# Optimization experiments

Hardware: AMD Instinct MI355X
Metric: run time of the kernel (lower is better)

Reference implementation:

```python
import jax, jax.numpy as jnp
import numpy as np

N, E, H, L, IN, OUT = 50000, 800000, 64, 14, 128, 112
MSG_EPS = 1e-7   # GENConv message epsilon
LN_EPS = 1e-5    # torch.nn.LayerNorm default eps


def setup_inputs() -> dict:
    key = jax.random.key(0)
    ks = jax.random.split(key, 8)
    s = 0.05
    x = jax.random.normal(ks[0], (N, IN), jnp.float32)
    edge_index = jax.random.randint(ks[1], (2, E), 0, N, dtype=jnp.int64)
    enc_W = jax.random.normal(ks[2], (IN, H), jnp.float32) * s
    enc_b = jnp.zeros((H,), jnp.float32)
    ln_g = jnp.ones((L, H), jnp.float32)
    ln_b = jnp.zeros((L, H), jnp.float32)
    mlp_W = jax.random.normal(ks[3], (L, H, H), jnp.float32) * s
    mlp_b = jnp.zeros((L, H), jnp.float32)
    pred_W = jax.random.normal(ks[4], (H, OUT), jnp.float32) * s
    pred_b = jnp.zeros((OUT,), jnp.float32)
    return dict(x=x, edge_index=edge_index, enc_W=enc_W, enc_b=enc_b,
                ln_g=ln_g, ln_b=ln_b, mlp_W=mlp_W, mlp_b=mlp_b,
                pred_W=pred_W, pred_b=pred_b)


def _layernorm(h, g, b):
    mu = jnp.mean(h, axis=-1, keepdims=True)
    var = jnp.mean(jnp.square(h - mu), axis=-1, keepdims=True)  # biased, as torch
    return (h - mu) * jax.lax.rsqrt(var + LN_EPS) * g + b


def _genconv(h, src, dst, W, b):
    # GENConv: msg = relu(x_src) + eps; softmax aggregation (t=1) over dst; out = Linear(x + agg)
    msg = jax.nn.relu(h[src]) + MSG_EPS                    # [E, H]
    mmax = jax.ops.segment_max(msg, dst, num_segments=N)   # [N, H]
    mmax = jnp.where(jnp.isfinite(mmax), mmax, 0.0)         # empty segments
    ex = jnp.exp(msg - mmax[dst])                           # [E, H]
    denom = jax.ops.segment_sum(ex, dst, num_segments=N)    # [N, H]
    num = jax.ops.segment_sum(msg * ex, dst, num_segments=N)
    agg = num / jnp.maximum(denom, 1e-16)                   # 0 for isolated nodes
    return (h + agg) @ W + b


def reference(x, edge_index, enc_W, enc_b, ln_g, ln_b, mlp_W, mlp_b, pred_W, pred_b):
    src, dst = edge_index[0], edge_index[1]
    h = x @ enc_W + enc_b                       # node feature encoder
    h = _genconv(h, src, dst, mlp_W[0], mlp_b[0])  # first GCN (no pre-norm in res+)

    def body(h, params):
        g, bl, W, b = params
        h2 = jax.nn.relu(_layernorm(h, g, bl))  # dropout is identity (eval)
        h = _genconv(h2, src, dst, W, b) + h    # residual
        return h, None

    h, _ = jax.lax.scan(body, h, (ln_g[:L - 1], ln_b[:L - 1], mlp_W[1:], mlp_b[1:]))
    return h @ pred_W + pred_b
```

## Files before the change

### kernel.cpp

```cpp
#include <hip/hip_runtime.h>
#include <hip/hip_bf16.h>

#define NN 50000
#define EE 800000
#define HD 64
#define LL 14
#define IND 128
#define OUTD 112
#define LN2 0.69314718056f

typedef __attribute__((ext_vector_type(8))) short short8;
typedef __attribute__((ext_vector_type(4))) float float4_;
typedef __attribute__((ext_vector_type(4))) unsigned short ushort4_;

__device__ __forceinline__ short bf16_hi(float x) {
    return (short)(__float_as_uint(x) >> 16);
}
__device__ __forceinline__ float bf16_f(short s) {
    return __uint_as_float(((unsigned)(unsigned short)s) << 16);
}
__device__ __forceinline__ float us2f(unsigned short u) {
    return __uint_as_float(((unsigned)u) << 16);
}
__device__ __forceinline__ unsigned short f2b_rne(float x) {
    unsigned u = __float_as_uint(x);
    u += 0x7fffu + ((u >> 16) & 1u);
    return (unsigned short)(u >> 16);
}

__device__ __forceinline__ void split8(const float* p, short8& hi, short8& lo) {
    float4_ a = *(const float4_*)p;
    float4_ b = *(const float4_*)(p + 4);
    float v[8] = {a[0], a[1], a[2], a[3], b[0], b[1], b[2], b[3]};
    #pragma unroll
    for (int j = 0; j < 8; ++j) {
        short h = bf16_hi(v[j]);
        hi[j] = h;
        lo[j] = bf16_hi(v[j] - bf16_f(h));
    }
}

__device__ __forceinline__ void load_b(const float* __restrict__ W, int ldw,
                                       int colbase, int krow, short8& hi, short8& lo) {
    #pragma unroll
    for (int j = 0; j < 8; ++j) {
        float wv = W[(krow + j) * ldw + colbase];
        short h = bf16_hi(wv);
        hi[j] = h;
        lo[j] = bf16_hi(wv - bf16_f(h));
    }
}

__device__ __forceinline__ float4_ mm3(short8 ah, short8 al, short8 bh, short8 bl,
                                       float4_ acc) {
    acc = __builtin_amdgcn_mfma_f32_16x16x32_bf16(ah, bh, acc, 0, 0, 0);
    acc = __builtin_amdgcn_mfma_f32_16x16x32_bf16(al, bh, acc, 0, 0, 0);
    acc = __builtin_amdgcn_mfma_f32_16x16x32_bf16(ah, bl, acc, 0, 0, 0);
    return acc;
}


__global__ void k_hist(const int* __restrict__ ei, int* __restrict__ cnt,
                       int* __restrict__ rank) {
    int e = blockIdx.x * blockDim.x + threadIdx.x;
    if (e < EE) rank[e] = atomicAdd(&cnt[ei[EE + e]], 1);
}

__global__ __launch_bounds__(1024) void k_scan1(const int* __restrict__ deg,
                                                int* __restrict__ excl,
                                                int* __restrict__ bsum) {
    __shared__ int ws[16];
    int tid = threadIdx.x, lane = tid & 63, w = tid >> 6;
    int gid = blockIdx.x * 1024 + tid;
    int v = (gid < NN) ? deg[gid] : 0;
    int x = v;
    #pragma unroll
    for (int d = 1; d < 64; d <<= 1) {
        int y = __shfl_up(x, d);
        if (lane >= d) x += y;
    }
    if (lane == 63) ws[w] = x;
    __syncthreads();
    if (tid == 0) {
        int acc = 0;
        for (int i = 0; i < 16; i++) { int t = ws[i]; ws[i] = acc; acc += t; }
        bsum[blockIdx.x] = acc;
    }
    __syncthreads();
    if (gid < NN) excl[gid] = x - v + ws[w];
}

__global__ void k_scan2(const int* __restrict__ bsum, int* __restrict__ boff, int nb) {
    if (threadIdx.x == 0) {
        int acc = 0;
        for (int i = 0; i < nb; i++) { boff[i] = acc; acc += bsum[i]; }
    }
}

__global__ __launch_bounds__(1024) void k_scan3(int* __restrict__ rp,
                                                const int* __restrict__ boff) {
    int gid = blockIdx.x * 1024 + threadIdx.x;
    if (gid < NN) rp[gid] += boff[blockIdx.x];
    if (gid == 0) rp[NN] = EE;
}

__global__ void k_scatter(const int* __restrict__ ei, const int* __restrict__ rp,
                          const int* __restrict__ rank, int* __restrict__ csrc) {
    int e = blockIdx.x * blockDim.x + threadIdx.x;
    if (e < EE) {
        int d = ei[EE + e];
        csrc[rp[d] + rank[e]] = ei[e];
    }
}


__global__ __launch_bounds__(256) void k_enc(const float* __restrict__ x,
                                             const float* __restrict__ W,
                                             const float* __restrict__ b,
                                             float* __restrict__ h,
                                             unsigned short* __restrict__ P0) {
    __shared__ float X[16 * 132];
    int tid = threadIdx.x, lane = tid & 63, w = tid >> 6;
    int nb = blockIdx.x * 16;
    int nq = lane >> 4, nr = lane & 15;
    int colbase = w * 16 + nr;

    {
        const float* src = x + (size_t)nb * IND + tid * 8;
        float4_ a = *(const float4_*)src;
        float4_ c = *(const float4_*)(src + 4);
        int m = tid >> 4, k8 = 8 * (tid & 15);
        *(float4_*)&X[m * 132 + k8] = a;
        *(float4_*)&X[m * 132 + k8 + 4] = c;
    }
    __syncthreads();

    float4_ acc = {};
    #pragma unroll
    for (int t = 0; t < 4; ++t) {
        short8 ah, al, bh, bl;
        split8(&X[nr * 132 + t * 32 + nq * 8], ah, al);
        load_b(W, HD, colbase, t * 32 + nq * 8, bh, bl);
        acc = mm3(ah, al, bh, bl, acc);
    }

    float bias = b[colbase];
    #pragma unroll
    for (int r = 0; r < 4; ++r) {
        int node = nb + nq * 4 + r;
        float y = acc[r] + bias;
        h[node * HD + colbase] = y;
        float msg = fminf(fmaxf(y, 0.f) + 1e-7f, 50.f);
        P0[node * HD + colbase] = f2b_rne(__expf(msg));
    }
}


__global__ __launch_bounds__(256) void k_layer(const unsigned short* __restrict__ Pin,
                                               const float* __restrict__ selfh,
                                               const float* __restrict__ hres,
                                               float* __restrict__ hout,
                                               unsigned short* __restrict__ Pout,
                                               const int* __restrict__ rp,
                                               const int* __restrict__ csrc,
                                               const float* __restrict__ W,
                                               const float* __restrict__ b,
                                               const float* __restrict__ gnext,
                                               const float* __restrict__ bnext) {
    __shared__ float T[16 * 68];
    int tid = threadIdx.x, lane = tid & 63, w = tid >> 6;
    int nb = blockIdx.x * 16;
    int nq = lane >> 4, nr = lane & 15;
    int colbase = w * 16 + nr;

    short8 Bhi[2], Blo[2];
    #pragma unroll
    for (int t = 0; t < 2; ++t)
        load_b(W, HD, colbase, t * 32 + nq * 8, Bhi[t], Blo[t]);

    #pragma unroll 1
    for (int i = 0; i < 4; ++i) {
        int node = nb + w * 4 + i;
        int beg = rp[node], end = rp[node + 1], deg = end - beg;
        float s = 0.f, n = 0.f;
        for (int chunk = 0; chunk < deg; chunk += 64) {
            int cnt = min(64, deg - chunk);
            int myidx = 0;
            if (chunk + lane < deg) myidx = csrc[beg + chunk + lane];
            int k = 0;
            for (; k + 16 <= cnt; k += 16) {
                unsigned short us[16];
                #pragma unroll
                for (int j = 0; j < 16; ++j) {
                    int src = __builtin_amdgcn_readlane(myidx, k + j);
                    us[j] = Pin[(src << 6) + lane];
                }
                #pragma unroll
                for (int j = 0; j < 16; ++j) {
                    float p = us2f(us[j]);
                    s += p;
                    n = fmaf(p, __log2f(p), n);
                }
            }
            for (; k + 4 <= cnt; k += 4) {
                unsigned short us[4];
                #pragma unroll
                for (int j = 0; j < 4; ++j) {
                    int src = __builtin_amdgcn_readlane(myidx, k + j);
                    us[j] = Pin[(src << 6) + lane];
                }
                #pragma unroll
                for (int j = 0; j < 4; ++j) {
                    float p = us2f(us[j]);
                    s += p;
                    n = fmaf(p, __log2f(p), n);
                }
            }
            for (; k < cnt; ++k) {
                int src = __builtin_amdgcn_readlane(myidx, k);
                float p = us2f(Pin[(src << 6) + lane]);
                s += p;
                n = fmaf(p, __log2f(p), n);
            }
        }
        float agg = LN2 * n / fmaxf(s, 1e-16f);
        float xv;
        if (selfh) {
            xv = selfh[node * HD + lane] + agg;
        } else {
            float ps = us2f(Pin[(node << 6) + lane]);
            xv = LN2 * __log2f(ps) - 1e-7f + agg;
        }
        T[(w * 4 + i) * 68 + lane] = xv;
    }
    __syncthreads();

    short8 Ahi[2], Alo[2];
    #pragma unroll
    for (int t = 0; t < 2; ++t)
        split8(&T[nr * 68 + t * 32 + nq * 8], Ahi[t], Alo[t]);
    __syncthreads();

    float4_ acc = {};
    #pragma unroll
    for (int t = 0; t < 2; ++t)
        acc = mm3(Ahi[t], Alo[t], Bhi[t], Blo[t], acc);

    float bias = b[colbase];
    #pragma unroll
    for (int r = 0; r < 4; ++r) {
        int m = nq * 4 + r;
        int node = nb + m;
        float v = acc[r] + bias;
        if (hres) v += hres[node * HD + colbase];
        hout[node * HD + colbase] = v;
        T[m * 68 + colbase] = v;
    }
    if (!Pout) return;
    __syncthreads();

    int m = tid >> 4, c4 = (tid & 15) * 4;
    float4_ vv = *(const float4_*)&T[m * 68 + c4];
    float ps_ = (vv[0] + vv[1]) + (vv[2] + vv[3]);
    float pq_ = (vv[0] * vv[0] + vv[1] * vv[1]) + (vv[2] * vv[2] + vv[3] * vv[3]);
    #pragma unroll
    for (int d = 8; d; d >>= 1) {
        ps_ += __shfl_xor(ps_, d);
        pq_ += __shfl_xor(pq_, d);
    }
    float mu = ps_ * (1.f / 64.f);
    float var = pq_ * (1.f / 64.f) - mu * mu;
    float inv = rsqrtf(fmaxf(var, 0.f) + 1e-5f);
    float4_ g4 = *(const float4_*)&gnext[c4];
    float4_ b4 = *(const float4_*)&bnext[c4];
    ushort4_ po;
    #pragma unroll
    for (int j = 0; j < 4; ++j) {
        float y = fmaxf((vv[j] - mu) * inv * g4[j] + b4[j], 0.f);
        float msg = fminf(y + 1e-7f, 50.f);
        po[j] = f2b_rne(__expf(msg));
    }
    *(ushort4_*)&Pout[(nb + m) * HD + c4] = po;
}


__global__ __launch_bounds__(256) void k_pred(const float* __restrict__ h,
                                              const float* __restrict__ W,
                                              const float* __restrict__ b,
                                              float* __restrict__ out) {
    __shared__ float T[16 * 68];
    int tid = threadIdx.x, lane = tid & 63, w = tid >> 6;
    int nb = blockIdx.x * 16;
    int nq = lane >> 4, nr = lane & 15;

    {
        const float* src = h + (size_t)nb * HD + tid * 4;
        float4_ a = *(const float4_*)src;
        int m = tid >> 4, k4 = 4 * (tid & 15);
        *(float4_*)&T[m * 68 + k4] = a;
    }
    __syncthreads();

    short8 Ahi[2], Alo[2];
    #pragma unroll
    for (int t = 0; t < 2; ++t)
        split8(&T[nr * 68 + t * 32 + nq * 8], Ahi[t], Alo[t]);

    for (int tt = w; tt < 7; tt += 4) {
        int colbase = tt * 16 + nr;
        float4_ acc = {};
        #pragma unroll
        for (int t = 0; t < 2; ++t) {
            short8 bh, bl;
            load_b(W, OUTD, colbase, t * 32 + nq * 8, bh, bl);
            acc = mm3(Ahi[t], Alo[t], bh, bl, acc);
        }
        float bias = b[colbase];
        #pragma unroll
        for (int r = 0; r < 4; ++r) {
            int node = nb + nq * 4 + r;
            out[node * OUTD + colbase] = acc[r] + bias;
        }
    }
}


extern "C" void kernel_launch(void* const* d_in, const int* in_sizes, int n_in,
                              void* d_out, int out_size, void* d_ws, size_t ws_size,
                              hipStream_t stream) {
    const float* x    = (const float*)d_in[0];
    const int*   ei   = (const int*)d_in[1];
    const float* encW = (const float*)d_in[2];
    const float* encb = (const float*)d_in[3];
    const float* lng  = (const float*)d_in[4];
    const float* lnb  = (const float*)d_in[5];
    const float* mlpW = (const float*)d_in[6];
    const float* mlpb = (const float*)d_in[7];
    const float* pW   = (const float*)d_in[8];
    const float* pb   = (const float*)d_in[9];
    float* out = (float*)d_out;

    float* hA  = (float*)d_ws;
    float* hB  = hA + (size_t)NN * HD;
    unsigned short* PA = (unsigned short*)(hB + (size_t)NN * HD);
    unsigned short* PB = PA + (size_t)NN * HD;
    int* rp   = (int*)(PB + (size_t)NN * HD);
    int* cnt  = rp + (NN + 1);
    int* csrc = cnt + NN;
    int* rank = csrc + EE;
    int* bsum = rank + EE;
    int* boff = bsum + 64;

    hipMemsetAsync(cnt, 0, NN * sizeof(int), stream);
    k_hist<<<(EE + 255) / 256, 256, 0, stream>>>(ei, cnt, rank);
    const int NB = (NN + 1023) / 1024;
    k_scan1<<<NB, 1024, 0, stream>>>(cnt, rp, bsum);
    k_scan2<<<1, 64, 0, stream>>>(bsum, boff, NB);
    k_scan3<<<NB, 1024, 0, stream>>>(rp, boff);
    k_scatter<<<(EE + 255) / 256, 256, 0, stream>>>(ei, rp, rank, csrc);

    k_enc<<<NN / 16, 256, 0, stream>>>(x, encW, encb, hA, PA);

    k_layer<<<NN / 16, 256, 0, stream>>>(PA, hA, nullptr, hB, PB, rp, csrc,
                                         mlpW, mlpb, lng, lnb);

    float* hres = hB;
    float* hdst = hA;
    unsigned short* pc = PB;
    unsigned short* pn = PA;
    for (int l = 1; l < LL; ++l) {
        bool last = (l == LL - 1);
        k_layer<<<NN / 16, 256, 0, stream>>>(pc, nullptr, hres, hdst,
                                             last ? nullptr : pn,
                                             rp, csrc,
                                             mlpW + (size_t)l * HD * HD,
                                             mlpb + (size_t)l * HD,
                                             last ? nullptr : lng + (size_t)l * HD,
                                             last ? nullptr : lnb + (size_t)l * HD);
        float* t = hres; hres = hdst; hdst = t;
        unsigned short* u = pc; pc = pn; pn = u;
    }

    k_pred<<<NN / 16, 256, 0, stream>>>(hres, pW, pb, out);
}
```

Before: 757.4 us.

## Gather four edges per wave with 8-byte loads per lane in aggregation

Restructures the neighbor gather so each wave handles four edges at once. Each 16-lane group loads one source row as two 32-bit words per lane, covering four bf16 features, instead of one 2-byte load per lane per edge. Partial sums are then reduced across groups with xor shuffles and written as float4. This aims to cut the number of load instructions and make memory accesses wider. The cost is shuffle reductions, per-iteration masking of tail edges, and a clamp before log2 so masked zeros stay finite.

Result: faster. 736.2 us (-2.8%).

```diff
diff --git a/kernel.cpp b/kernel.cpp
--- a/kernel.cpp
+++ b/kernel.cpp
@@ -178,60 +178,63 @@
     for (int t = 0; t < 2; ++t)
         load_b(W, HD, colbase, t * 32 + nq * 8, Bhi[t], Blo[t]);
 
+    int g = lane >> 4;
+    int ci = lane & 15;
     #pragma unroll 1
     for (int i = 0; i < 4; ++i) {
         int node = nb + w * 4 + i;
         int beg = rp[node], end = rp[node + 1], deg = end - beg;
-        float s = 0.f, n = 0.f;
+        float s0 = 0.f, s1 = 0.f, s2 = 0.f, s3 = 0.f;
+        float n0 = 0.f, n1 = 0.f, n2 = 0.f, n3 = 0.f;
         for (int chunk = 0; chunk < deg; chunk += 64) {
             int cnt = min(64, deg - chunk);
             int myidx = 0;
             if (chunk + lane < deg) myidx = csrc[beg + chunk + lane];
-            int k = 0;
-            for (; k + 16 <= cnt; k += 16) {
-                unsigned short us[16];
-                #pragma unroll
-                for (int j = 0; j < 16; ++j) {
-                    int src = __builtin_amdgcn_readlane(myidx, k + j);
-                    us[j] = Pin[(src << 6) + lane];
-                }
-                #pragma unroll
-                for (int j = 0; j < 16; ++j) {
-                    float p = us2f(us[j]);
-                    s += p;
-                    n = fmaf(p, __log2f(p), n);
-                }
+            int nb4 = (cnt + 3) >> 2;
+            #pragma unroll 2
+            for (int k = 0; k < nb4; ++k) {
+                int src = __shfl(myidx, k * 4 + g);
+                const unsigned* pp = (const unsigned*)(Pin + ((size_t)src << 6)) + ci * 2;
+                unsigned d0 = pp[0], d1 = pp[1];
+                if (k * 4 + g >= cnt) { d0 = 0u; d1 = 0u; }
+                float p0 = __uint_as_float(d0 << 16);
+                float p1 = __uint_as_float(d0 & 0xffff0000u);
+                float p2 = __uint_as_float(d1 << 16);
+                float p3 = __uint_as_float(d1 & 0xffff0000u);
+                s0 += p0; s1 += p1; s2 += p2; s3 += p3;
+                n0 = fmaf(p0, __log2f(fmaxf(p0, 1e-20f)), n0);
+                n1 = fmaf(p1, __log2f(fmaxf(p1, 1e-20f)), n1);
+                n2 = fmaf(p2, __log2f(fmaxf(p2, 1e-20f)), n2);
+                n3 = fmaf(p3, __log2f(fmaxf(p3, 1e-20f)), n3);
             }
-            for (; k + 4 <= cnt; k += 4) {
-                unsigned short us[4];
-                #pragma unroll
-                for (int j = 0; j < 4; ++j) {
-                    int src = __builtin_amdgcn_readlane(myidx, k + j);
-                    us[j] = Pin[(src << 6) + lane];
-                }
-                #pragma unroll
-                for (int j = 0; j < 4; ++j) {
-                    float p = us2f(us[j]);
-                    s += p;
-                    n = fmaf(p, __log2f(p), n);
-                }
+        }
+        #pragma unroll
+        for (int d = 16; d < 64; d <<= 1) {
+            s0 += __shfl_xor(s0, d); s1 += __shfl_xor(s1, d);
+            s2 += __shfl_xor(s2, d); s3 += __shfl_xor(s3, d);
+            n0 += __shfl_xor(n0, d); n1 += __shfl_xor(n1, d);
+            n2 += __shfl_xor(n2, d); n3 += __shfl_xor(n3, d);
+        }
+        if (g == 0) {
+            float a0 = LN2 * n0 / fmaxf(s0, 1e-16f);
+            float a1 = LN2 * n1 / fmaxf(s1, 1e-16f);
+            float a2 = LN2 * n2 / fmaxf(s2, 1e-16f);
+            float a3 = LN2 * n3 / fmaxf(s3, 1e-16f);
+            float4_ xv;
+            if (selfh) {
+                float4_ sf = *(const float4_*)&selfh[(size_t)node * HD + ci * 4];
+                xv[0] = sf[0] + a0; xv[1] = sf[1] + a1;
+                xv[2] = sf[2] + a2; xv[3] = sf[3] + a3;
+            } else {
+                const unsigned* pp = (const unsigned*)(Pin + ((size_t)node << 6)) + ci * 2;
+                unsigned d0 = pp[0], d1 = pp[1];
+                xv[0] = LN2 * __log2f(__uint_as_float(d0 << 16)) - 1e-7f + a0;
+                xv[1] = LN2 * __log2f(__uint_as_float(d0 & 0xffff0000u)) - 1e-7f + a1;
+                xv[2] = LN2 * __log2f(__uint_as_float(d1 << 16)) - 1e-7f + a2;
+                xv[3] = LN2 * __log2f(__uint_as_float(d1 & 0xffff0000u)) - 1e-7f + a3;
             }
-            for (; k < cnt; ++k) {
-                int src = __builtin_amdgcn_readlane(myidx, k);
-                float p = us2f(Pin[(src << 6) + lane]);
-                s += p;
-                n = fmaf(p, __log2f(p), n);
-            }
-        }
-        float agg = LN2 * n / fmaxf(s, 1e-16f);
-        float xv;
-        if (selfh) {
-            xv = selfh[node * HD + lane] + agg;
-        } else {
-            float ps = us2f(Pin[(node << 6) + lane]);
-            xv = LN2 * __log2f(ps) - 1e-7f + agg;
-        }
-        T[(w * 4 + i) * 68 + lane] = xv;
+            *(float4_*)&T[(w * 4 + i) * 68 + ci * 4] = xv;
+        }
     }
     __syncthreads();
 
```
